# Performance work log

Measured on AMD Instinct MI355X. Metric: run time of the kernel, lower is better.

Reference implementation:

```python
import jax, jax.numpy as jnp
import numpy as np

# Model dims (from DecoderLSTM defaults)
H = 512       # hidden_size
E = 128       # embedding_dim == input_size
NC = 27       # num_class (output_size)
NE = 28       # num_embeddings = num_class + 1
B = 256       # batch
T = 512       # timesteps


def setup_inputs() -> dict:
    key = jax.random.key(0)
    ks = jax.random.split(key, 12)
    s = 0.05
    return {
        "target_inputs": jax.random.randint(ks[0], (B, T), 0, NE),
        "target_lengths": jax.random.randint(ks[1], (B,), 1, T + 1),
        "h0": jax.random.normal(ks[2], (4, B, H), dtype=jnp.float32),   # [num_layer*num_dirs, B, H]
        "c0": jax.random.normal(ks[3], (4, B, H), dtype=jnp.float32),
        "embed": jax.random.normal(ks[4], (NE, E), dtype=jnp.float32) * s,
        "Wih0": jax.random.normal(ks[5], (2, 4 * H, E), dtype=jnp.float32) * s,      # layer0 [dir,4H,E]
        "Wih1": jax.random.normal(ks[6], (2, 4 * H, 2 * H), dtype=jnp.float32) * s,  # layer1 [dir,4H,2H]
        "Whh": jax.random.normal(ks[7], (2, 2, 4 * H, H), dtype=jnp.float32) * s,    # [layer,dir,4H,H]
        "bih": jax.random.normal(ks[8], (2, 2, 4 * H), dtype=jnp.float32) * s,
        "bhh": jax.random.normal(ks[9], (2, 2, 4 * H), dtype=jnp.float32) * s,
        "Wout": jax.random.normal(ks[10], (NC, 2 * H), dtype=jnp.float32) * s,
        "bout": jax.random.normal(ks[11], (NC,), dtype=jnp.float32) * s,
    }


def _lstm_cell(x, h, c, Wih, Whh, b):
    # x: [B,in], h/c: [B,H]; PyTorch gate order i,f,g,o
    g = x @ Wih.T + h @ Whh.T + b
    i, f, gg, o = jnp.split(g, 4, axis=-1)
    c2 = jax.nn.sigmoid(f) * c + jax.nn.sigmoid(i) * jnp.tanh(gg)
    h2 = jax.nn.sigmoid(o) * jnp.tanh(c2)
    return h2, c2


def reference(target_inputs, target_lengths, h0, c0, embed,
              Wih0, Wih1, Whh, bih, bhh, Wout, bout):
    b = bih + bhh                              # [layer,dir,4H]
    x_emb = embed[target_inputs]               # [B,T,E]
    seq_len = target_inputs.shape[1]

    def step(carry, xt):
        h, c = carry                           # [4,B,H] each; layout layer*2+dir
        hf, cf = _lstm_cell(xt, h[0], c[0], Wih0[0], Whh[0, 0], b[0, 0])
        hb, cb = _lstm_cell(xt, h[1], c[1], Wih0[1], Whh[0, 1], b[0, 1])
        y0 = jnp.concatenate([hf, hb], axis=-1)                 # [B,2H]
        h2f, c2f = _lstm_cell(y0, h[2], c[2], Wih1[0], Whh[1, 0], b[1, 0])
        h2b, c2b = _lstm_cell(y0, h[3], c[3], Wih1[1], Whh[1, 1], b[1, 1])
        y1 = jnp.concatenate([h2f, h2b], axis=-1)               # [B,2H]
        hn = jnp.stack([hf, hb, h2f, h2b])
        cn = jnp.stack([cf, cb, c2f, c2b])
        return (hn, cn), y1 @ Wout.T + bout                      # logits [B,NC]

    _, logits_t = jax.lax.scan(step, (h0, c0), jnp.swapaxes(x_emb, 0, 1))
    logits = jnp.swapaxes(logits_t, 0, 1)                        # [B,T,NC]
    mask = jnp.arange(seq_len)[None, :] < target_lengths[:, None]
    outputs = jnp.where(mask[:, :, None], logits, jnp.zeros((), logits.dtype))
    return outputs, target_lengths
```

## Files before the change

### kernel.cpp

```cpp
#include <hip/hip_runtime.h>
#include <hip/hip_bf16.h>
#include <stdint.h>

typedef unsigned short ushort_t;
typedef unsigned char u8_t;
typedef unsigned long long u64_t;

#define H   512
#define E   128
#define NC  27
#define NE  28
#define B   256
#define T   512
#define FH  2048
#define NPH (T + 2)
#define NL0 64
#define NL1 128
#define NOUT 32
#define BHs (B * H)
#define WOFF_L0 131072
#define WOFF_L1 65536
#define LDS_BYTES (160 * 1024)
#define CROW 256

typedef __bf16 bf16x8 __attribute__((ext_vector_type(8)));
typedef float  f32x4  __attribute__((ext_vector_type(4)));

#define WAITV(n) asm volatile("s_waitcnt vmcnt(" #n ")" ::: "memory")
#define LADDER8(rem) do { if ((rem) >= 7) WAITV(7); else if ((rem) == 6) WAITV(6); \
                          else if ((rem) == 5) WAITV(5); else if ((rem) == 4) WAITV(4); \
                          else if ((rem) == 3) WAITV(3); else if ((rem) == 2) WAITV(2); \
                          else if ((rem) == 1) WAITV(1); else WAITV(0); } while (0)

__device__ __forceinline__ ushort_t f2b(float x) {
    uint32_t u = __float_as_uint(x);
    uint32_t r = (u + 0x7FFFu + ((u >> 16) & 1u)) >> 16;
    return (ushort_t)r;
}
__device__ __forceinline__ u8_t f2fp8(float x) {
    uint32_t u = __float_as_uint(x);
    uint32_t s = (u >> 24) & 0x80u;
    int E8 = (int)((u >> 23) & 0xffu);
    uint32_t M = u & 0x7fffffu;
    if (E8 == 0) return (u8_t)s;
    int e8 = E8 - 120;
    uint32_t code;
    if (e8 <= 0) {
        int sh = 1 - e8;
        if (sh > 23) return (u8_t)s;
        code = (0x800000u | M) >> sh;
    } else {
        code = ((uint32_t)e8 << 23) | M;
    }
    uint32_t r = (code + 0x7ffffu + ((code >> 20) & 1u)) >> 20;
    if (r > 0x7eu) r = 0x7eu;
    return (u8_t)(s | r);
}
__device__ __forceinline__ float sigm(float x) {
    return 1.f / (1.f + __expf(-x));
}
__device__ __forceinline__ void stc1(u8_t* p, u8_t v) {
    __hip_atomic_store(p, v, __ATOMIC_RELAXED, __HIP_MEMORY_SCOPE_AGENT);
}
__device__ __forceinline__ void stc2(ushort_t* p, ushort_t v) {
    __hip_atomic_store(p, v, __ATOMIC_RELAXED, __HIP_MEMORY_SCOPE_AGENT);
}
__device__ __forceinline__ void stc4f(float* p, float v) {
    __hip_atomic_store(p, v, __ATOMIC_RELAXED, __HIP_MEMORY_SCOPE_AGENT);
}
__device__ __forceinline__ bf16x8 ldc16(const ushort_t* p) {
    union { u64_t q[2]; bf16x8 v; } u;
    u.q[0] = __hip_atomic_load((const u64_t*)p,       __ATOMIC_RELAXED, __HIP_MEMORY_SCOPE_AGENT);
    u.q[1] = __hip_atomic_load(((const u64_t*)p) + 1, __ATOMIC_RELAXED, __HIP_MEMORY_SCOPE_AGENT);
    return u.v;
}
__device__ __forceinline__ void gload_lds16c(const void* g, void* l) {
    __builtin_amdgcn_global_load_lds(
        (const __attribute__((address_space(1))) void*)g,
        (__attribute__((address_space(3))) void*)l, 16, 0, 17);
}

__device__ __forceinline__ void stageA8(const u8_t* __restrict__ hsrc, int k0,
                                        char* chunk, int wave, int lane) {
    int gd = lane & 3;
    #pragma unroll
    for (int i = 0; i < 2; ++i) {
        int r = wave * 32 + i * 16 + (lane >> 2);
        int fr = (r & 3) ^ ((r >> 2) & 3);
        const u8_t* g = hsrc + (size_t)r * H + k0 + ((gd ^ fr) << 4);
        gload_lds16c((const void*)g, (void*)(chunk + wave * 2048 + i * 1024));
    }
}

__device__ __forceinline__ void stageB8(const u8_t* __restrict__ hsrc, int rb, int k0,
                                        char* chunk, int wave, int lane) {
    int r = wave * 16 + (lane >> 2);
    int gd = lane & 3;
    int fr = (r & 3) ^ ((r >> 2) & 3);
    const u8_t* g = hsrc + (size_t)(rb + r) * H + k0 + ((gd ^ fr) << 4);
    gload_lds16c((const void*)g, (void*)(chunk + wave * 1024));
}


__global__ void k_init(int* __restrict__ cnt) {
    for (int i = blockIdx.x * blockDim.x + threadIdx.x; i < 3 * NPH * CROW;
         i += gridDim.x * blockDim.x) cnt[i] = 0;
}

__global__ void k_g0(const float* __restrict__ embed, const float* __restrict__ Wih0,
                     const float* __restrict__ bih, const float* __restrict__ bhh,
                     float* __restrict__ G0, float* __restrict__ bias1) {
    int i = blockIdx.x * blockDim.x + threadIdx.x;
    if (i < 2 * NE * FH) {
        int d = i / (NE * FH);
        int rem = i % (NE * FH);
        int e = rem / FH;
        int n = rem % FH;
        int g = n >> 9, j = n & 511;
        const float* er = embed + (size_t)e * E;
        const float* wr = Wih0 + ((size_t)d * FH + n) * E;
        float s = 0.f;
        #pragma unroll 8
        for (int k = 0; k < E; ++k) s += er[k] * wr[k];
        G0[(((size_t)d * NE + e) * 512 + j) * 4 + g]
            = s + bih[(size_t)d * FH + n] + bhh[(size_t)d * FH + n];
    }
    if (i < 2 * FH) bias1[i] = bih[2 * FH + i] + bhh[2 * FH + i];
}

__global__ void k_state(const float* __restrict__ h0, ushort_t* __restrict__ hb16,
                        u8_t* __restrict__ hf8) {
    int i = blockIdx.x * blockDim.x + threadIdx.x;
    if (i >= 4 * B * H) return;
    int cell = i / (B * H);
    int rem  = i % (B * H);
    hb16[((size_t)(cell * 3 + 2)) * BHs + rem] = f2b(h0[i]);
    hf8 [((size_t)(cell * 3 + 2)) * BHs + rem] = f2fp8(h0[i]);
}

__global__ void k_tokT(const int* __restrict__ tok, int* __restrict__ tokT) {
    int i = blockIdx.x * blockDim.x + threadIdx.x;
    if (i < B * T) {
        int b = i / T, t = i % T;
        tokT[(size_t)t * B + b] = tok[i];
    }
}

__global__ void k_len(const int* __restrict__ lens, float* __restrict__ out_len) {
    int i = threadIdx.x;
    if (i < B) out_len[i] = (float)lens[i];
}

__device__ __forceinline__ int polled(const int* c) {
    int t = 0;
    #pragma unroll
    for (int i = 0; i < 16; ++i)
        t += __hip_atomic_load(c + i * 16, __ATOMIC_RELAXED, __HIP_MEMORY_SCOPE_AGENT);
    return t;
}

__device__ __forceinline__ void boundary(int* cntL0, int* cntL1, int* cntOUT,
                                         int role, int bid, int p) {
    __syncthreads();
    if (threadIdx.x == 0) {
        int* mine = (role == 0) ? cntL0 : (role == 1) ? cntL1 : cntOUT;
        __hip_atomic_fetch_add(mine + p * CROW + (bid & 15) * 16, 1,
                               __ATOMIC_RELAXED, __HIP_MEMORY_SCOPE_AGENT);
        const int q = p + 1;
        int nl0 = -1, nl1 = -1, nou = -1;
        if (role == 0) {
            if (q < T) {
                nl0 = q - 1;
                if (q >= 2) nl1 = q - 2;
            }
        } else if (role == 1) {
            if (q >= 1 && q <= T) {
                nl0 = q - 1;
                if (q >= 2) { nl1 = q - 1; nou = q - 2; }
            }
        } else {
            if (q >= 2) nl1 = q - 1;
        }
        for (;;) {
            int a = (nl0 >= 0) ? polled(cntL0 + nl0 * CROW) : NL0;
            int b = (nl1 >= 0) ? polled(cntL1 + nl1 * CROW) : NL1;
            int c = (nou >= 0) ? polled(cntOUT + nou * CROW) : NOUT;
            if (a >= NL0 && b >= NL1 && c >= NOUT) break;
            __builtin_amdgcn_s_sleep(2);
        }
    }
    __syncthreads();
    __builtin_amdgcn_sched_barrier(0);
}

__global__ __launch_bounds__(512, 2) void k_persist(
    const float* __restrict__ Whh, const float* __restrict__ Wih1,
    const float* __restrict__ G0, const float* __restrict__ bias1,
    const float* __restrict__ c0, ushort_t* __restrict__ hb16,
    u8_t* __restrict__ hf8,
    const int* __restrict__ tokT, const int* __restrict__ lens,
    const float* __restrict__ Wout, const float* __restrict__ bout,
    float* __restrict__ out, int* __restrict__ cnt)
{
    extern __shared__ char smem[];
    const int bid = blockIdx.x;
    const int tid = threadIdx.x;
    const int lane = tid & 63, wave = tid >> 6;
    const int lrow = lane & 15, kg = lane >> 4;
    const int row0 = wave * 32;
    const int sw8 = lrow & 7;

    int* cntL0  = cnt;
    int* cntL1  = cnt + NPH * CROW;
    int* cntOUT = cnt + 2 * NPH * CROW;
    const int role = (bid < NL0) ? 0 : (bid < NL0 + NL1) ? 1 : 2;

    int wksoff[2];
    #pragma unroll
    for (int ks = 0; ks < 2; ++ks)
        wksoff[ks] = (((ks * 4 + kg) ^ sw8) << 3);

    if (bid < 64) {
        const int cell = bid >> 5, jt = bid & 31, j0 = jt * 16;
        const float* Wsrc = Whh + (size_t)cell * FH * H;
        for (int r = wave; r < 64; r += 8) {
            int grow = (r >> 4) * 512 + j0 + (r & 15);
            const float* src = Wsrc + (size_t)grow * H;
            for (int c = lane; c < H; c += 64) {
                int slot = c >> 3;
                int ssw = (slot & ~7) | ((slot ^ r) & 7);
                *(u8_t*)(smem + WOFF_L0 + r * 512 + ssw * 8 + (c & 7)) = f2fp8(src[c]);
            }
        }
    } else if (bid < 192) {
        const int q = bid - 64;
        const int rem = q & 63, cell = 2 + (rem >> 5), jt = rem & 31, j0 = jt * 16;
        const float* Wi = Wih1 + (size_t)(cell - 2) * FH * (2 * H);
        const float* Wh = Whh + (size_t)cell * FH * H;
        for (int r = wave; r < 64; r += 8) {
            int grow = (r >> 4) * 512 + j0 + (r & 15);
            const float* si = Wi + (size_t)grow * (2 * H);
            const float* sh = Wh + (size_t)grow * H;
            for (int c = lane; c < 1536; c += 64) {
                float v = (c < 1024) ? si[c] : sh[c - 1024];
                int slot = c >> 3;
                int ssw = (slot & ~7) | ((slot ^ r) & 7);
                *(u8_t*)(smem + WOFF_L1 + r * 1536 + ssw * 8 + (c & 7)) = f2fp8(v);
            }
        }
    } else {
        for (int r = wave; r < NC; r += 8) {
            const float* src = Wout + (size_t)r * (2 * H);
            int sw = (r & 7) << 4;
            for (int c = lane; c < 2 * H; c += 64) {
                int byte = ((r * (2 * H) + c) * 2) ^ sw;
                *(ushort_t*)(smem + byte) = f2b(src[c]);
            }
        }
    }
    __syncthreads();

    if (bid < 64) {
        const int cell = bid >> 5, jt = bid & 31, j0 = jt * 16;
        const int j = j0 + lrow;
        const int fA = (lrow & 3) ^ ((lrow >> 2) & 3);
        int aoffK[2];
        #pragma unroll
        for (int ks = 0; ks < 2; ++ks)
            aoffK[ks] = (row0 + lrow) * 64 + ((((ks << 1) | (kg >> 1)) ^ fA) << 4) + ((kg & 1) << 3);
        int wgbase[4];
        #pragma unroll
        for (int g = 0; g < 4; ++g) wgbase[g] = WOFF_L0 + (g * 16 + lrow) * 512;

        float cv[8];
        #pragma unroll
        for (int i = 0; i < 8; ++i) {
            int bb = row0 + (i >> 2) * 16 + kg * 4 + (i & 3);
            cv[i] = c0[((size_t)cell * B + bb) * H + j];
        }
        f32x4 g0v[8];
        #pragma unroll
        for (int i = 0; i < 8; ++i) {
            int bb = row0 + (i >> 2) * 16 + kg * 4 + (i & 3);
            int tk = tokT[bb];
            g0v[i] = *(const f32x4*)(G0 + (((size_t)cell * NE + tk) * 512 + j) * 4);
        }

        for (int p = 0; p < NPH; ++p) {
            if (p < T) {
                const int pm3 = p % 3;
                const int parR = (pm3 + 2) % 3, parW = pm3;
                const u8_t* hsrc = hf8 + (size_t)(cell * 3 + parR) * BHs;

                #pragma unroll
                for (int c2 = 0; c2 < 8; ++c2)
                    stageA8(hsrc, c2 * 64, smem + c2 * 16384, wave, lane);

                f32x4 acc[2][4];
                #pragma unroll
                for (int m = 0; m < 2; ++m)
                    #pragma unroll
                    for (int g = 0; g < 4; ++g) acc[m][g] = (f32x4){0.f, 0.f, 0.f, 0.f};

                #pragma unroll
                for (int t = 0; t < 8; ++t) {
                    if (t == 0)      WAITV(14);
                    else if (t == 1) WAITV(12);
                    else if (t == 2) WAITV(10);
                    else if (t == 3) WAITV(8);
                    else if (t == 4) WAITV(6);
                    else if (t == 5) WAITV(4);
                    else if (t == 6) WAITV(2);
                    else             WAITV(0);
                    __builtin_amdgcn_sched_barrier(0);
                    const char* Ab = smem + t * 16384;
                    u64_t aA[2][2], wW[2][4];
                    #pragma unroll
                    for (int ks = 0; ks < 2; ++ks) {
                        aA[ks][0] = *(const u64_t*)(Ab + aoffK[ks]);
                        aA[ks][1] = *(const u64_t*)(Ab + aoffK[ks] + 1024);
                        #pragma unroll
                        for (int g = 0; g < 4; ++g)
                            wW[ks][g] = *(const u64_t*)(smem + wgbase[g] + t * 64 + wksoff[ks]);
                    }
                    asm volatile("s_waitcnt lgkmcnt(0)" ::: "memory");
                    __builtin_amdgcn_sched_barrier(0);
                    #pragma unroll
                    for (int ks = 0; ks < 2; ++ks)
                        #pragma unroll
                        for (int g = 0; g < 4; ++g) {
                            acc[0][g] = __builtin_amdgcn_mfma_f32_16x16x32_fp8_fp8(
                                (long)aA[ks][0], (long)wW[ks][g], acc[0][g], 0, 0, 0);
                            acc[1][g] = __builtin_amdgcn_mfma_f32_16x16x32_fp8_fp8(
                                (long)aA[ks][1], (long)wW[ks][g], acc[1][g], 0, 0, 0);
                        }
                }

                #pragma unroll
                for (int i = 0; i < 8; ++i) {
                    int mf = i >> 2, r = i & 3;
                    int bb = row0 + mf * 16 + kg * 4 + r;
                    float gi = acc[mf][0][r] + g0v[i][0];
                    float gf = acc[mf][1][r] + g0v[i][1];
                    float gg = acc[mf][2][r] + g0v[i][2];
                    float go = acc[mf][3][r] + g0v[i][3];
                    float ii = sigm(gi), ff = sigm(gf), oo = sigm(go);
                    float tg = tanhf(gg);
                    float cn = ff * cv[i] + ii * tg;
                    cv[i] = cn;
                    float hn = oo * tanhf(cn);
                    stc1(&hf8[((size_t)(cell * 3 + parW) * B + bb) * H + j], f2fp8(hn));
                }
                if (p + 1 < T) {
                    #pragma unroll
                    for (int i = 0; i < 8; ++i) {
                        int bb = row0 + (i >> 2) * 16 + kg * 4 + (i & 3);
                        int tk = tokT[(size_t)(p + 1) * B + bb];
                        g0v[i] = *(const f32x4*)(G0 + (((size_t)cell * NE + tk) * 512 + j) * 4);
                    }
                }
            }
            if (p < NPH - 1) boundary(cntL0, cntL1, cntOUT, role, bid, p);
        }
    } else if (bid < 192) {
        const int q = bid - 64;
        const int bt = q >> 6, rem = q & 63;
        const int cell = 2 + (rem >> 5), jt = rem & 31;
        const int j0 = jt * 16, rb = bt * 128;
        const int j = j0 + lrow;
        const int fB = (lrow & 3) ^ ((wave * 4 + (lrow >> 2)) & 3);
        int aoffB[2];
        #pragma unroll
        for (int ks = 0; ks < 2; ++ks)
            aoffB[ks] = (wave * 16 + lrow) * 64 + ((((ks << 1) | (kg >> 1)) ^ fB) << 4) + ((kg & 1) << 3);
        int wgbase[4];
        #pragma unroll
        for (int g = 0; g < 4; ++g) wgbase[g] = WOFF_L1 + (g * 16 + lrow) * 1536;

        float b1v[4];
        #pragma unroll
        for (int g = 0; g < 4; ++g) b1v[g] = bias1[(size_t)(cell - 2) * FH + g * 512 + j];

        float cv[4];
        #pragma unroll
        for (int r = 0; r < 4; ++r) {
            int bb = rb + wave * 16 + kg * 4 + r;
            cv[r] = c0[((size_t)cell * B + bb) * H + j];
        }

        for (int p = 0; p < NPH; ++p) {
            if (p >= 1 && p <= T) {
                const int pm3 = p % 3;
                const int parY  = (pm3 + 2) % 3;
                const int parR2 = (pm3 + 1) % 3;
                const int parW  = parY;
                const u8_t* base0 = hf8 + (size_t)(0 * 3 + parY) * BHs;
                const u8_t* base1 = hf8 + (size_t)(1 * 3 + parY) * BHs;
                const u8_t* base2 = hf8 + (size_t)(cell * 3 + parR2) * BHs;

                #pragma unroll
                for (int c2 = 0; c2 < 8; ++c2)
                    stageB8(base0, rb, c2 * 64, smem + c2 * 8192, wave, lane);

                f32x4 acc[4];
                #pragma unroll
                for (int g = 0; g < 4; ++g) acc[g] = (f32x4){0.f, 0.f, 0.f, 0.f};

                #pragma unroll
                for (int t = 0; t < 24; ++t) {
                    LADDER8(23 - t);
                    __builtin_amdgcn_sched_barrier(0);
                    const char* Ab = smem + (t & 7) * 8192;
                    u64_t aA[2], wW[2][4];
                    #pragma unroll
                    for (int ks = 0; ks < 2; ++ks) {
                        aA[ks] = *(const u64_t*)(Ab + aoffB[ks]);
                        #pragma unroll
                        for (int g = 0; g < 4; ++g)
                            wW[ks][g] = *(const u64_t*)(smem + wgbase[g] + t * 64 + wksoff[ks]);
                    }
                    asm volatile("s_waitcnt lgkmcnt(0)" ::: "memory");
                    __builtin_amdgcn_sched_barrier(0);
                    if (t + 8 < 24) {
                        int c2 = t + 8;
                        const u8_t* src = (c2 < 16) ? base1 : base2;
                        stageB8((c2 < 16) ? base1 : base2, rb, (c2 & 7) * 64,
                                smem + (t & 7) * 8192, wave, lane);
                        (void)src;
                    }
                    __builtin_amdgcn_sched_barrier(0);
                    #pragma unroll
                    for (int ks = 0; ks < 2; ++ks)
                        #pragma unroll
                        for (int g = 0; g < 4; ++g)
                            acc[g] = __builtin_amdgcn_mfma_f32_16x16x32_fp8_fp8(
                                (long)aA[ks], (long)wW[ks][g], acc[g], 0, 0, 0);
                }

                #pragma unroll
                for (int r = 0; r < 4; ++r) {
                    int bb = rb + wave * 16 + kg * 4 + r;
                    float gi = acc[0][r] + b1v[0];
                    float gf = acc[1][r] + b1v[1];
                    float gg = acc[2][r] + b1v[2];
                    float go = acc[3][r] + b1v[3];
                    float ii = sigm(gi), ff = sigm(gf), oo = sigm(go);
                    float tg = tanhf(gg);
                    float cn = ff * cv[r] + ii * tg;
                    cv[r] = cn;
                    float hn = oo * tanhf(cn);
                    size_t hi = ((size_t)(cell * 3 + parW) * B + bb) * H + j;
                    stc1(&hf8[hi], f2fp8(hn));
                    stc2(&hb16[hi], f2b(hn));
                }
            }
            if (p < NPH - 1) boundary(cntL0, cntL1, cntOUT, role, bid, p);
        }
    } else {
        const int b = (bid - 192) * 8 + wave;
        const int c = lane & 31, kh = lane >> 5;
        const int half = lane >> 5, qq = lane & 31;
        const int sww = (c & 7) << 4;
        const int rowbase = c * 2048;
        const int lenb = lens[b];
        const float bo = (c < NC) ? bout[c] : 0.f;
        char* scr = smem + 57344 + wave * 2048;

        for (int p = 0; p < NPH; ++p) {
            if (p >= 2) {
                const int t2 = p - 2;
                const int parL = (p % 3 + 1) % 3;
                {
                    const ushort_t* src = hb16 + (size_t)((2 + half) * 3 + parL) * BHs
                                        + (size_t)b * H + qq * 16;
                    bf16x8 v0 = ldc16(src);
                    bf16x8 v1 = ldc16(src + 8);
                    char* dst = scr + half * 1024 + qq * 32;
                    *(bf16x8*)dst = v0;
                    *(bf16x8*)(dst + 16) = v1;
                }
                __syncthreads();
                float sum = 0.f;
                if (c < NC) {
                    const char* ybase = scr + kh * 1024;
                    #pragma unroll 8
                    for (int t = 0; t < 64; ++t) {
                        bf16x8 v = *(const bf16x8*)(ybase + t * 16);
                        bf16x8 w = *(const bf16x8*)(smem + rowbase + ((kh * 1024 + t * 16) ^ sww));
                        #pragma unroll
                        for (int i = 0; i < 8; ++i) sum += (float)v[i] * (float)w[i];
                    }
                }
                sum += __shfl_xor(sum, 32);
                if (kh == 0 && c < NC) {
                    float val = (t2 < lenb) ? (sum + bo) : 0.f;
                    stc4f(&out[((size_t)b * T + t2) * NC + c], val);
                }
            }
            if (p < NPH - 1) boundary(cntL0, cntL1, cntOUT, role, bid, p);
        }
    }
}


extern "C" void kernel_launch(void* const* d_in, const int* in_sizes, int n_in,
                              void* d_out, int out_size, void* d_ws, size_t ws_size,
                              hipStream_t stream) {
    const int*   tok   = (const int*)d_in[0];
    const int*   lens  = (const int*)d_in[1];
    const float* h0    = (const float*)d_in[2];
    const float* c0    = (const float*)d_in[3];
    const float* embed = (const float*)d_in[4];
    const float* Wih0  = (const float*)d_in[5];
    const float* Wih1  = (const float*)d_in[6];
    const float* Whh   = (const float*)d_in[7];
    const float* bih   = (const float*)d_in[8];
    const float* bhh   = (const float*)d_in[9];
    const float* Wout  = (const float*)d_in[10];
    const float* bout  = (const float*)d_in[11];
    float* out = (float*)d_out;

    ushort_t* hb16  = (ushort_t*)d_ws;
    u8_t*     hf8   = (u8_t*)(hb16 + (size_t)4 * 3 * B * H);
    float*    G0    = (float*)(hf8 + (size_t)4 * 3 * B * H);
    float*    bias1 = G0 + 2 * NE * FH;
    int*      cnt   = (int*)(bias1 + 2 * FH);
    int*      tokT  = cnt + 3 * NPH * CROW;

    (void)hipFuncSetAttribute((const void*)k_persist,
                              hipFuncAttributeMaxDynamicSharedMemorySize, LDS_BYTES);

    k_init<<<256, 256, 0, stream>>>(cnt);
    k_g0<<<(2 * NE * FH + 255) / 256, 256, 0, stream>>>(embed, Wih0, bih, bhh, G0, bias1);
    k_state<<<(4 * B * H + 255) / 256, 256, 0, stream>>>(h0, hb16, hf8);
    k_tokT<<<(B * T + 255) / 256, 256, 0, stream>>>(tok, tokT);
    k_len<<<1, 256, 0, stream>>>(lens, out + (size_t)B * T * NC);

    k_persist<<<NL0 + NL1 + NOUT, 512, LDS_BYTES, stream>>>(
        Whh, Wih1, G0, bias1, c0, hb16, hf8, tokT, lens, Wout, bout, out, cnt);
}
```

Baseline: 5.150 ms.

## Split layer-1 barrier to overlap layer-0 input GEMM with recurrent wait

```diff
diff --git a/kernel.cpp b/kernel.cpp
--- a/kernel.cpp
+++ b/kernel.cpp
@@ -167,29 +167,39 @@
         __hip_atomic_fetch_add(mine + p * CROW + (bid & 15) * 16, 1,
                                __ATOMIC_RELAXED, __HIP_MEMORY_SCOPE_AGENT);
         const int q = p + 1;
-        int nl0 = -1, nl1 = -1, nou = -1;
+        int nl0 = -1, nl1 = -1;
         if (role == 0) {
             if (q < T) {
                 nl0 = q - 1;
                 if (q >= 2) nl1 = q - 2;
             }
         } else if (role == 1) {
-            if (q >= 1 && q <= T) {
-                nl0 = q - 1;
-                if (q >= 2) { nl1 = q - 1; nou = q - 2; }
-            }
+            if (q >= 1 && q <= T) nl0 = q - 1;
         } else {
             if (q >= 2) nl1 = q - 1;
         }
         for (;;) {
             int a = (nl0 >= 0) ? polled(cntL0 + nl0 * CROW) : NL0;
             int b = (nl1 >= 0) ? polled(cntL1 + nl1 * CROW) : NL1;
-            int c = (nou >= 0) ? polled(cntOUT + nou * CROW) : NOUT;
-            if (a >= NL0 && b >= NL1 && c >= NOUT) break;
+            if (a >= NL0 && b >= NL1) break;
             __builtin_amdgcn_s_sleep(2);
         }
     }
     __syncthreads();
+    __builtin_amdgcn_sched_barrier(0);
+}
+
+__device__ __forceinline__ void gateL1(const int* cntL1, const int* cntOUT, int p) {
+    __builtin_amdgcn_sched_barrier(0);
+    if (threadIdx.x == 0) {
+        for (;;) {
+            int a = polled(cntL1 + (p - 1) * CROW);
+            int b = (p >= 2) ? polled(cntOUT + (p - 2) * CROW) : NOUT;
+            if (a >= NL1 && b >= NOUT) break;
+            __builtin_amdgcn_s_sleep(2);
+        }
+    }
+    __builtin_amdgcn_s_barrier();
     __builtin_amdgcn_sched_barrier(0);
 }
 
@@ -398,17 +408,17 @@
                 const u8_t* base1 = hf8 + (size_t)(1 * 3 + parY) * BHs;
                 const u8_t* base2 = hf8 + (size_t)(cell * 3 + parR2) * BHs;
 
+                f32x4 acc[4];
+                #pragma unroll
+                for (int g = 0; g < 4; ++g) acc[g] = (f32x4){0.f, 0.f, 0.f, 0.f};
+
                 #pragma unroll
                 for (int c2 = 0; c2 < 8; ++c2)
                     stageB8(base0, rb, c2 * 64, smem + c2 * 8192, wave, lane);
 
-                f32x4 acc[4];
-                #pragma unroll
-                for (int g = 0; g < 4; ++g) acc[g] = (f32x4){0.f, 0.f, 0.f, 0.f};
-
-                #pragma unroll
-                for (int t = 0; t < 24; ++t) {
-                    LADDER8(23 - t);
+                #pragma unroll
+                for (int t = 0; t < 16; ++t) {
+                    LADDER8(15 - t);
                     __builtin_amdgcn_sched_barrier(0);
                     const char* Ab = smem + (t & 7) * 8192;
                     u64_t aA[2], wW[2][4];
@@ -421,13 +431,38 @@
                     }
                     asm volatile("s_waitcnt lgkmcnt(0)" ::: "memory");
                     __builtin_amdgcn_sched_barrier(0);
-                    if (t + 8 < 24) {
-                        int c2 = t + 8;
-                        const u8_t* src = (c2 < 16) ? base1 : base2;
-                        stageB8((c2 < 16) ? base1 : base2, rb, (c2 & 7) * 64,
-                                smem + (t & 7) * 8192, wave, lane);
-                        (void)src;
+                    if (t < 8)
+                        stageB8(base1, rb, t * 64, smem + (t & 7) * 8192, wave, lane);
+                    __builtin_amdgcn_sched_barrier(0);
+                    #pragma unroll
+                    for (int ks = 0; ks < 2; ++ks)
+                        #pragma unroll
+                        for (int g = 0; g < 4; ++g)
+                            acc[g] = __builtin_amdgcn_mfma_f32_16x16x32_fp8_fp8(
+                                (long)aA[ks], (long)wW[ks][g], acc[g], 0, 0, 0);
+                }
+
+                gateL1(cntL1, cntOUT, p);
+
+                #pragma unroll
+                for (int c2 = 0; c2 < 8; ++c2)
+                    stageB8(base2, rb, c2 * 64, smem + c2 * 8192, wave, lane);
+
+                #pragma unroll
+                for (int tt = 0; tt < 8; ++tt) {
+                    const int t = 16 + tt;
+                    LADDER8(7 - tt);
+                    __builtin_amdgcn_sched_barrier(0);
+                    const char* Ab = smem + (tt & 7) * 8192;
+                    u64_t aA[2], wW[2][4];
+                    #pragma unroll
+                    for (int ks = 0; ks < 2; ++ks) {
+                        aA[ks] = *(const u64_t*)(Ab + aoffB[ks]);
+                        #pragma unroll
+                        for (int g = 0; g < 4; ++g)
+                            wW[ks][g] = *(const u64_t*)(smem + wgbase[g] + t * 64 + wksoff[ks]);
                     }
+                    asm volatile("s_waitcnt lgkmcnt(0)" ::: "memory");
                     __builtin_amdgcn_sched_barrier(0);
                     #pragma unroll
                     for (int ks = 0; ks < 2; ++ks)
```

After: 4.697 ms, median of 2. 8.8% less time.
